# Kernel tuning notes

Measured on AMD Instinct MI355X. Metric: run time of the kernel, lower is better.

## Reference

```python
import jax, jax.numpy as jnp
import numpy as np


def setup_inputs() -> dict:
    key = jax.random.key(0)
    ks = jax.random.split(key, 16)
    B, C, H, W = 2, 64, 512, 512
    Nl, Nr = 100000, 20000

    def lin(k, fan_in, fan_out):
        kw, kb = jax.random.split(k)
        bound = 1.0 / np.sqrt(fan_in)
        w = jax.random.uniform(kw, (fan_in, fan_out), jnp.float32, -bound, bound)
        b = jax.random.uniform(kb, (fan_out,), jnp.float32, -bound, bound)
        return w, b

    w_lin, b_lin = lin(ks[0], 128, 64)
    w1, b1 = lin(ks[1], 128, 64)
    w2, b2 = lin(ks[2], 64, 32)
    w3, b3 = lin(ks[3], 32, 16)
    w4, b4 = lin(ks[4], 16, 1)

    return {
        "pc0_map": jax.random.normal(ks[5], (B, C, H, W), jnp.float32),
        "pc1_map": jax.random.normal(ks[6], (B, C, H, W), jnp.float32),
        "flow_map": jax.random.normal(ks[7], (B, C, H, W), jnp.float32),
        "lidar_coords": jax.random.randint(ks[8], (B, Nl, 3), 0, 512).astype(jnp.int64),
        "radar_coords": jax.random.randint(ks[9], (B, Nr, 3), 0, 512).astype(jnp.int64),
        "w_lin": w_lin, "b_lin": b_lin,
        "w1": w1, "b1": b1, "w2": w2, "b2": b2,
        "w3": w3, "b3": b3, "w4": w4, "b4": b4,
    }


def reference(pc0_map, pc1_map, flow_map, lidar_coords, radar_coords,
              w_lin, b_lin, w1, b1, w2, b2, w3, b3, w4, b4):
    gelu = lambda x: jax.nn.gelu(x, approximate=False)  # torch nn.GELU default (erf)

    def seg_single(p0, p1, fl, lc, rc):
        # lc: [Nl,3], rc: [Nr,3]; cat(lidar, radar) for all three maps
        coords = jnp.concatenate([lc, rc], axis=0)        # [N,3]
        r, c = coords[:, 1], coords[:, 2]
        f0 = p0[:, r, c].T                                # [N,64]
        f1 = p1[:, r, c].T                                # [N,64]
        ff = fl[:, r, c].T                                # [N,64]
        pc = jnp.concatenate([f0, f1], axis=1) @ w_lin + b_lin   # [N,64]
        h = jnp.concatenate([pc, ff], axis=1)             # [N,128]
        h = gelu(h @ w1 + b1)
        h = gelu(h @ w2 + b2)
        h = gelu(h @ w3 + b3)
        s = jax.nn.sigmoid(h @ w4 + b4)                   # [N,1]
        return s[:, 0]

    # [B, Nl+Nr] stacked (original returns a per-batch list; fixed N lets us stack)
    return jax.vmap(seg_single)(pc0_map, pc1_map, flow_map, lidar_coords, radar_coords)
```

## Files before the change

kernel.cpp:

```cpp
#include <hip/hip_runtime.h>
#include <math.h>

#define NPTS 120000
#define NLID 100000
#define NRAD 20000
#define NTOT (2 * NPTS)
#define MAPW 512
#define MAPHW (512 * 512)
#define NBINS 16384

typedef short sh8 __attribute__((ext_vector_type(8)));
typedef float f32x4 __attribute__((ext_vector_type(4)));
typedef unsigned short u16;

#define FSTR 200
#define H1S 72
#define H2S 40
#define H3S 24

__device__ __forceinline__ float gelu_f(float x) {
    return 0.5f * x * (1.0f + erff(x * 0.7071067811865476f));
}
__device__ __forceinline__ u16 f2bf(float f) {
    unsigned int u = __float_as_uint(f);
    return (u16)((u + 0x7FFFu + ((u >> 16) & 1u)) >> 16);
}
__device__ __forceinline__ float bf2f(u16 h) {
    return __uint_as_float((unsigned int)h << 16);
}

__device__ __forceinline__ void point_rc(int p, const int* __restrict__ lidar,
                                         const int* __restrict__ radar,
                                         int& b, int& r, int& c) {
    b = p / NPTS;
    int i = p - b * NPTS;
    if (i < NLID) {
        const int* cd = lidar + (size_t)(b * NLID + i) * 3;
        r = cd[1]; c = cd[2];
    } else {
        const int* cd = radar + (size_t)(b * NRAD + (i - NLID)) * 3;
        r = cd[1]; c = cd[2];
    }
}
__device__ __forceinline__ int bin_key(int b, int r, int c) {
    return (b << 13) | (r << 4) | (c >> 5);
}
__global__ void hist_kernel(const int* __restrict__ lidar, const int* __restrict__ radar,
                            int* __restrict__ hist) {
    int p = blockIdx.x * blockDim.x + threadIdx.x;
    if (p >= NTOT) return;
    int b, r, c; point_rc(p, lidar, radar, b, r, c);
    atomicAdd(&hist[bin_key(b, r, c)], 1);
}
__global__ __launch_bounds__(1024) void scan_kernel(const int* __restrict__ hist,
                                                    int* __restrict__ offs) {
    __shared__ int sums[1024];
    const int t = threadIdx.x;
    int local[16]; int s = 0;
    #pragma unroll
    for (int i = 0; i < 16; i++) { local[i] = hist[t * 16 + i]; s += local[i]; }
    sums[t] = s;
    __syncthreads();
    for (int off = 1; off < 1024; off <<= 1) {
        int add = (t >= off) ? sums[t - off] : 0;
        __syncthreads();
        sums[t] += add;
        __syncthreads();
    }
    int excl = (t == 0) ? 0 : sums[t - 1];
    #pragma unroll
    for (int i = 0; i < 16; i++) { offs[t * 16 + i] = excl; excl += local[i]; }
}
__global__ void scatter_kernel(const int* __restrict__ lidar, const int* __restrict__ radar,
                               int* __restrict__ offs, int2* __restrict__ sorted) {
    int p = blockIdx.x * blockDim.x + threadIdx.x;
    if (p >= NTOT) return;
    int b, r, c; point_rc(p, lidar, radar, b, r, c);
    int pos = atomicAdd(&offs[bin_key(b, r, c)], 1);
    sorted[pos] = make_int2(p, (r << 9) | c);
}

__global__ void wprep_kernel(const float* __restrict__ w_lin, const float* __restrict__ b_lin,
                             const float* __restrict__ w1, const float* __restrict__ b1,
                             const float* __restrict__ w2, const float* __restrict__ w3,
                             u16* __restrict__ wfrag1, u16* __restrict__ wfrag2,
                             u16* __restrict__ wfrag3, float* __restrict__ b_eff) {
    int e = blockIdx.x * blockDim.x + threadIdx.x;
    if (e < 12288) {
        int fi = e >> 9, r = e & 511, lane = r >> 3, j = r & 7;
        int kk = fi >> 2, nt = fi & 3;
        int k = kk * 32 + (lane >> 4) * 8 + j;
        int n = nt * 16 + (lane & 15);
        float val;
        if (k < 128) {
            float s = 0.f;
            for (int jj = 0; jj < 64; jj++) s += w_lin[k * 64 + jj] * w1[jj * 64 + n];
            val = s;
        } else {
            val = w1[(k - 64) * 64 + n];
        }
        wfrag1[e] = f2bf(val);
    } else if (e < 12288 + 2048) {
        int e2 = e - 12288;
        int fi = e2 >> 9, lane = (e2 >> 3) & 63, j = e2 & 7;
        int kk = fi >> 1, nt = fi & 1;
        int k = kk * 32 + (lane >> 4) * 8 + j;
        int n = nt * 16 + (lane & 15);
        wfrag2[e2] = f2bf(w2[k * 32 + n]);
    } else if (e < 12288 + 2048 + 512) {
        int e3 = e - 12288 - 2048;
        int lane = e3 >> 3, j = e3 & 7;
        int k = (lane >> 4) * 8 + j;
        int n = lane & 15;
        wfrag3[e3] = f2bf(w3[k * 16 + n]);
    } else if (e < 12288 + 2048 + 512 + 64) {
        int n = e - 12288 - 2048 - 512;
        float s = b1[n];
        for (int jj = 0; jj < 64; jj++) s += b_lin[jj] * w1[jj * 64 + n];
        b_eff[n] = s;
    }
}

__global__ __launch_bounds__(256) void fbseg_kernel(
    const float* __restrict__ p0, const float* __restrict__ p1,
    const float* __restrict__ fl,
    const int2* __restrict__ sorted,
    const u16* __restrict__ wfrag1, const u16* __restrict__ wfrag2,
    const u16* __restrict__ wfrag3, const float* __restrict__ b_eff,
    const float* __restrict__ b2, const float* __restrict__ b3,
    const float* __restrict__ w4, const float* __restrict__ b4,
    float* __restrict__ out)
{
    __shared__ __align__(16) u16 smem[21504];
    u16* feat = smem;
    u16* H1   = smem + 64 * FSTR;
    u16* H2   = H1 + 4 * 16 * H1S;
    u16* H3   = H2 + 4 * 16 * H2S;

    const int tid = threadIdx.x;
    const int p_base = blockIdx.x * 64;

    {
        const int pt = tid & 63;
        const int cs = tid >> 6;
        const int2 e = sorted[p_base + pt];
        const int b = e.x / NPTS;
        const int r = (e.y >> 9) & 511;
        const int c = e.y & 511;
        const size_t base = (size_t)b * ((size_t)64 * MAPHW) + (size_t)r * MAPW + (size_t)c;
        const float* maps[3] = {p0 + base, p1 + base, fl + base};
        #pragma unroll
        for (int m = 0; m < 3; m++) {
            const float* mp = maps[m];
            float v[16];
            #pragma unroll
            for (int u = 0; u < 16; u++) v[u] = mp[(size_t)(cs + u * 4) * MAPHW];
            #pragma unroll
            for (int u = 0; u < 16; u++) feat[pt * FSTR + m * 64 + cs + u * 4] = f2bf(v[u]);
        }
    }
    __syncthreads();

    const int wv = tid >> 6;
    const int lane = tid & 63;
    const int m0 = wv * 16;
    const int lr = lane & 15;
    const int lq = lane >> 4;

    f32x4 acc1[4] = {};
    #pragma unroll
    for (int kk = 0; kk < 6; kk++) {
        sh8 a = *(const sh8*)&feat[(m0 + lr) * FSTR + kk * 32 + lq * 8];
        #pragma unroll
        for (int nt = 0; nt < 4; nt++) {
            sh8 bfr = *(const sh8*)(wfrag1 + ((kk * 4 + nt) * 64 + lane) * 8);
            acc1[nt] = __builtin_amdgcn_mfma_f32_16x16x32_bf16(a, bfr, acc1[nt], 0, 0, 0);
        }
    }
    u16* H1w = H1 + wv * 16 * H1S;
    #pragma unroll
    for (int nt = 0; nt < 4; nt++) {
        const int n = nt * 16 + lr;
        const float bias = b_eff[n];
        #pragma unroll
        for (int rg = 0; rg < 4; rg++) {
            const int row = lq * 4 + rg;
            H1w[row * H1S + n] = f2bf(gelu_f(acc1[nt][rg] + bias));
        }
    }

    f32x4 acc2[2] = {};
    #pragma unroll
    for (int kk = 0; kk < 2; kk++) {
        sh8 a = *(const sh8*)&H1w[lr * H1S + kk * 32 + lq * 8];
        #pragma unroll
        for (int nt = 0; nt < 2; nt++) {
            sh8 bfr = *(const sh8*)(wfrag2 + ((kk * 2 + nt) * 64 + lane) * 8);
            acc2[nt] = __builtin_amdgcn_mfma_f32_16x16x32_bf16(a, bfr, acc2[nt], 0, 0, 0);
        }
    }
    u16* H2w = H2 + wv * 16 * H2S;
    #pragma unroll
    for (int nt = 0; nt < 2; nt++) {
        const int n = nt * 16 + lr;
        const float bias = b2[n];
        #pragma unroll
        for (int rg = 0; rg < 4; rg++) {
            const int row = lq * 4 + rg;
            H2w[row * H2S + n] = f2bf(gelu_f(acc2[nt][rg] + bias));
        }
    }

    f32x4 acc3 = {};
    {
        sh8 a = *(const sh8*)&H2w[lr * H2S + lq * 8];
        sh8 bfr = *(const sh8*)(wfrag3 + lane * 8);
        acc3 = __builtin_amdgcn_mfma_f32_16x16x32_bf16(a, bfr, acc3, 0, 0, 0);
    }
    u16* H3w = H3 + wv * 16 * H3S;
    {
        const float bias = b3[lr];
        #pragma unroll
        for (int rg = 0; rg < 4; rg++) {
            const int row = lq * 4 + rg;
            H3w[row * H3S + lr] = f2bf(gelu_f(acc3[rg] + bias));
        }
    }

    if (lane < 16) {
        float s = b4[0];
        #pragma unroll
        for (int k = 0; k < 16; k++) s = fmaf(bf2f(H3w[lane * H3S + k]), w4[k], s);
        const int orig = sorted[p_base + m0 + lane].x;
        out[orig] = 1.0f / (1.0f + expf(-s));
    }
}

extern "C" void kernel_launch(void* const* d_in, const int* in_sizes, int n_in,
                              void* d_out, int out_size, void* d_ws, size_t ws_size,
                              hipStream_t stream) {
    const float* p0    = (const float*)d_in[0];
    const float* p1    = (const float*)d_in[1];
    const float* fl    = (const float*)d_in[2];
    const int*   lidar = (const int*)d_in[3];
    const int*   radar = (const int*)d_in[4];
    const float* w_lin = (const float*)d_in[5];
    const float* b_lin = (const float*)d_in[6];
    const float* w1    = (const float*)d_in[7];
    const float* b1    = (const float*)d_in[8];
    const float* w2    = (const float*)d_in[9];
    const float* b2    = (const float*)d_in[10];
    const float* w3    = (const float*)d_in[11];
    const float* b3    = (const float*)d_in[12];
    const float* w4    = (const float*)d_in[13];
    const float* b4    = (const float*)d_in[14];
    float* out = (float*)d_out;

    char* ws = (char*)d_ws;
    int*  hist   = (int*)ws;
    int*  offs   = (int*)(ws + NBINS * sizeof(int));
    int2* sorted = (int2*)(ws + 2 * NBINS * sizeof(int));
    char* wbase  = ws + 2 * NBINS * sizeof(int) + (size_t)NTOT * sizeof(int2);
    u16*  wfrag1 = (u16*)wbase;
    u16*  wfrag2 = (u16*)(wbase + 12288 * 2);
    u16*  wfrag3 = (u16*)(wbase + (12288 + 2048) * 2);
    float* b_eff = (float*)(wbase + (12288 + 2048 + 512) * 2);

    hipMemsetAsync(hist, 0, NBINS * sizeof(int), stream);
    hipLaunchKernelGGL(hist_kernel, dim3((NTOT + 255) / 256), dim3(256), 0, stream,
                       lidar, radar, hist);
    hipLaunchKernelGGL(scan_kernel, dim3(1), dim3(1024), 0, stream, hist, offs);
    hipLaunchKernelGGL(scatter_kernel, dim3((NTOT + 255) / 256), dim3(256), 0, stream,
                       lidar, radar, offs, sorted);
    hipLaunchKernelGGL(wprep_kernel, dim3((14912 + 255) / 256), dim3(256), 0, stream,
                       w_lin, b_lin, w1, b1, w2, w3, wfrag1, wfrag2, wfrag3, b_eff);
    hipLaunchKernelGGL(fbseg_kernel, dim3(NTOT / 64), dim3(256), 0, stream,
                       p0, p1, fl, sorted, wfrag1, wfrag2, wfrag3, b_eff,
                       b2, b3, w4, b4, out);
}
```

Measured before the change: 423.6 us.

## Gather features directly into LDS via global_load_lds and convert to bf16 at MFMA read

Replaces the register-staged gather plus bf16 conversion with asynchronous global_load_lds transfers that write fp32 features straight into a channel-major LDS tile (row stride 65 to avoid bank conflicts). The bf16 conversion moves to the point where the MFMA A operands are assembled, and the hidden-layer buffers reuse the same LDS region after an extra barrier. The aim is to cut VGPR pressure and instruction count in the memory-bound gather stage and to raise loads in flight. In exchange, LDS usage doubles to fp32 and the A-fragment build now does eight scalar LDS reads and conversions per operand.

```diff
diff --git a/kernel.cpp b/kernel.cpp
--- a/kernel.cpp
+++ b/kernel.cpp
@@ -12,11 +12,13 @@
 typedef short sh8 __attribute__((ext_vector_type(8)));
 typedef float f32x4 __attribute__((ext_vector_type(4)));
 typedef unsigned short u16;
-
-#define FSTR 200
+typedef unsigned int u32;
+
+#define FROW 65
 #define H1S 72
 #define H2S 40
 #define H3S 24
+#define HWAVE (16 * (H1S + H2S + H3S))
 
 __device__ __forceinline__ float gelu_f(float x) {
     return 0.5f * x * (1.0f + erff(x * 0.7071067811865476f));
@@ -131,53 +133,62 @@
     const float* __restrict__ w4, const float* __restrict__ b4,
     float* __restrict__ out)
 {
-    __shared__ __align__(16) u16 smem[21504];
-    u16* feat = smem;
-    u16* H1   = smem + 64 * FSTR;
-    u16* H2   = H1 + 4 * 16 * H1S;
-    u16* H3   = H2 + 4 * 16 * H2S;
+    __shared__ __align__(16) float smem[192 * FROW];
 
     const int tid = threadIdx.x;
+    const int wv = tid >> 6;
+    const int lane = tid & 63;
     const int p_base = blockIdx.x * 64;
 
     {
-        const int pt = tid & 63;
-        const int cs = tid >> 6;
-        const int2 e = sorted[p_base + pt];
+        const int2 e = sorted[p_base + lane];
         const int b = e.x / NPTS;
         const int r = (e.y >> 9) & 511;
         const int c = e.y & 511;
-        const size_t base = (size_t)b * ((size_t)64 * MAPHW) + (size_t)r * MAPW + (size_t)c;
-        const float* maps[3] = {p0 + base, p1 + base, fl + base};
+        const size_t off = (size_t)b * ((size_t)64 * MAPHW) + (size_t)r * MAPW + (size_t)c;
+        const float* bases[3] = {p0 + off, p1 + off, fl + off};
         #pragma unroll
         for (int m = 0; m < 3; m++) {
-            const float* mp = maps[m];
-            float v[16];
+            const float* gp = bases[m] + (size_t)wv * MAPHW;
             #pragma unroll
-            for (int u = 0; u < 16; u++) v[u] = mp[(size_t)(cs + u * 4) * MAPHW];
-            #pragma unroll
-            for (int u = 0; u < 16; u++) feat[pt * FSTR + m * 64 + cs + u * 4] = f2bf(v[u]);
+            for (int u = 0; u < 16; u++) {
+                const int chu = __builtin_amdgcn_readfirstlane(m * 64 + u * 4 + wv);
+                __builtin_amdgcn_global_load_lds(
+                    (const __attribute__((address_space(1))) u32*)gp,
+                    (__attribute__((address_space(3))) u32*)(&smem[chu * FROW]),
+                    4, 0, 0);
+                gp += (size_t)4 * MAPHW;
+            }
         }
     }
     __syncthreads();
 
-    const int wv = tid >> 6;
-    const int lane = tid & 63;
     const int m0 = wv * 16;
     const int lr = lane & 15;
     const int lq = lane >> 4;
+    const int col = m0 + lr;
 
     f32x4 acc1[4] = {};
     #pragma unroll
     for (int kk = 0; kk < 6; kk++) {
-        sh8 a = *(const sh8*)&feat[(m0 + lr) * FSTR + kk * 32 + lq * 8];
+        sh8 a;
+        u16* ap = (u16*)&a;
+        #pragma unroll
+        for (int j = 0; j < 8; j++)
+            ap[j] = f2bf(smem[(kk * 32 + lq * 8 + j) * FROW + col]);
         #pragma unroll
         for (int nt = 0; nt < 4; nt++) {
             sh8 bfr = *(const sh8*)(wfrag1 + ((kk * 4 + nt) * 64 + lane) * 8);
             acc1[nt] = __builtin_amdgcn_mfma_f32_16x16x32_bf16(a, bfr, acc1[nt], 0, 0, 0);
         }
     }
-    u16* H1w = H1 + wv * 16 * H1S;
+    __syncthreads();
+
+    u16* Hbase = (u16*)smem + wv * HWAVE;
+    u16* H1w = Hbase;
+    u16* H2w = Hbase + 16 * H1S;
+    u16* H3w = Hbase + 16 * H1S + 16 * H2S;
+
     #pragma unroll
     for (int nt = 0; nt < 4; nt++) {
         const int n = nt * 16 + lr;
@@ -199,7 +210,6 @@
             acc2[nt] = __builtin_amdgcn_mfma_f32_16x16x32_bf16(a, bfr, acc2[nt], 0, 0, 0);
         }
     }
-    u16* H2w = H2 + wv * 16 * H2S;
     #pragma unroll
     for (int nt = 0; nt < 2; nt++) {
         const int n = nt * 16 + lr;
@@ -217,7 +227,6 @@
         sh8 bfr = *(const sh8*)(wfrag3 + lane * 8);
         acc3 = __builtin_amdgcn_mfma_f32_16x16x32_bf16(a, bfr, acc3, 0, 0, 0);
     }
-    u16* H3w = H3 + wv * 16 * H3S;
     {
         const float bias = b3[lr];
         #pragma unroll
```

Result: no change. 422.9 us (-0.2%).
